# Kernel tuning notes

Measured on AMD Instinct MI355X. Metric: run time of the kernel, lower is better.

The kernel has to match this reference:

```python
import jax, jax.numpy as jnp
import numpy as np

DEGREE = 4  # standard ChebyKANLinear default -> 5 basis functions
LN_EPS = 1e-5


def cheby_basis(x, degree=DEGREE):
    # x: [N, D] -> basis [N, D, degree+1] of Chebyshev T_k(tanh(x))
    t = jnp.tanh(x)
    polys = [jnp.ones_like(t), t]
    for _ in range(2, degree + 1):
        polys.append(2.0 * t * polys[-1] - polys[-2])
    return jnp.stack(polys, axis=-1)


def cheby_kan_linear(x, coeffs):
    # coeffs: [in, out, degree+1]
    basis = cheby_basis(x)  # [N, in, degree+1]
    return jnp.einsum('nid,iod->no', basis, coeffs)


def layer_norm(x, gamma, beta):
    mu = jnp.mean(x, axis=-1, keepdims=True)
    var = jnp.mean(jnp.square(x - mu), axis=-1, keepdims=True)
    return (x - mu) * jax.lax.rsqrt(var + LN_EPS) * gamma + beta


def setup_inputs() -> dict:
    key = jax.random.key(0)
    ks = jax.random.split(key, 4)
    N, C, H = 262144, 128, 32
    scale1 = 1.0 / (C * (DEGREE + 1)) ** 0.5
    scale2 = 1.0 / (H * (DEGREE + 1)) ** 0.5
    return {
        'PRV_feat': jax.random.normal(ks[0], (N, C), dtype=jnp.float32),
        'PR_feat': jax.random.normal(ks[1], (N, C), dtype=jnp.float32),
        'coeffs1': jax.random.normal(ks[2], (C, H, DEGREE + 1), dtype=jnp.float32) * scale1,
        'ln_gamma': jnp.ones((H,), dtype=jnp.float32),
        'ln_beta': jnp.zeros((H,), dtype=jnp.float32),
        'coeffs2': jax.random.normal(ks[3], (H, 1, DEGREE + 1), dtype=jnp.float32) * scale2,
        'alpha': jnp.float32(0.5),
    }


def reference(PRV_feat, PR_feat, coeffs1, ln_gamma, ln_beta, coeffs2, alpha):
    # context encoder: ChebyKAN -> LayerNorm -> ReLU
    context = cheby_kan_linear(PR_feat, coeffs1)           # [N, H]
    context = jax.nn.relu(layer_norm(context, ln_gamma, ln_beta))
    # attention gate: ChebyKAN -> Sigmoid, [N, 1]
    attn = jax.nn.sigmoid(cheby_kan_linear(context, coeffs2))
    enhanced = PRV_feat * attn                              # broadcast over channels
    fused = alpha * enhanced + PRV_feat
    return fused
```

## Files before the change

### kernel.cpp

```cpp
#include <hip/hip_runtime.h>
#include <hip/hip_bf16.h>

#define C_DIM 128
#define H_DIM 32

typedef __attribute__((ext_vector_type(8))) short bf16x8;
typedef __attribute__((ext_vector_type(4))) float f32x4;

__device__ __forceinline__ float tanh_fast(float x) {
    float e = __expf(2.0f * x);
    return 1.0f - 2.0f * __builtin_amdgcn_rcpf(e + 1.0f);
}

__device__ __forceinline__ short f2bf(float f) {
    return __builtin_bit_cast(short, __float2bfloat16(f));
}

__global__ void prep_kernel(const float* __restrict__ c1, const float* __restrict__ c2,
                            unsigned short* __restrict__ Bpack, float* __restrict__ bias1,
                            float* __restrict__ E2, float* __restrict__ bias2) {
    const int tid = threadIdx.x;
    const int idx = blockIdx.x * 256 + tid;
    {
        int kc = idx >> 10;
        int oh = (idx >> 9) & 1;
        int l  = (idx >> 3) & 63;
        int j  = idx & 7;
        int g  = l >> 4;
        int kc2 = kc >> 1, kh = kc & 1;
        int c   = kc2 * 16 + 4 * g + 2 * kh + (j >> 2);
        int col = oh * 16 + (l & 15);
        int p   = j & 3;
        const float* cc = c1 + (c * H_DIM + col) * 5;
        float v = (p == 0) ? cc[1] - 3.0f * cc[3]
                : (p == 1) ? 2.0f * cc[2] - 8.0f * cc[4]
                : (p == 2) ? 4.0f * cc[3]
                           : 8.0f * cc[4];
        Bpack[idx] = (unsigned short)f2bf(v);
    }
    if (blockIdx.x == 0) {
        __shared__ float part[256];
        const int o = tid & 31, ch = tid >> 5;
        float b = 0.0f;
        for (int i = ch * 16; i < ch * 16 + 16; ++i) {
            const float* cc = c1 + (i * H_DIM + o) * 5;
            b += cc[0] - cc[2] + cc[4];
        }
        part[tid] = b;
        __syncthreads();
        if (tid < 32) {
            float s = 0.0f;
            #pragma unroll
            for (int k = 0; k < 8; ++k) s += part[k * 32 + tid];
            bias1[tid] = s;
            const float* cc = c2 + tid * 5;
            float4 e;
            e.x = cc[1] - 3.0f * cc[3];
            e.y = 2.0f * cc[2] - 8.0f * cc[4];
            e.z = 4.0f * cc[3];
            e.w = 8.0f * cc[4];
            reinterpret_cast<float4*>(E2)[tid] = e;
        }
        __syncthreads();
        if (tid < 32) part[tid] = c2[tid * 5] - c2[tid * 5 + 2] + c2[tid * 5 + 4];
        __syncthreads();
        if (tid == 0) {
            float b2 = 0.0f;
            for (int h = 0; h < 32; ++h) b2 += part[h];
            bias2[0] = b2;
        }
    }
}

__global__ __launch_bounds__(512, 4) void fused_kernel(
        const float* __restrict__ PRV, const float* __restrict__ PR,
        const unsigned short* __restrict__ Bpack, const float* __restrict__ bias1,
        const float* __restrict__ E2, const float* __restrict__ bias2,
        const float* __restrict__ gamma, const float* __restrict__ beta,
        const float* __restrict__ alphap, float* __restrict__ out) {
    __shared__ short sB[16 * 2 * 64 * 8];
    __shared__ float s_scale[256];

    const int tid  = threadIdx.x;
    const int wid  = tid >> 6;
    const int lane = tid & 63;
    const int g    = lane >> 4;
    const int lr   = lane & 15;

    const float4* pr4 = reinterpret_cast<const float4*>(PR);
    const size_t rbase = (size_t)blockIdx.x * 256 + wid * 32 + lr;
    const float4* q0 = pr4 + (rbase +  0) * (C_DIM / 4) + g;
    const float4* q1 = pr4 + (rbase + 16) * (C_DIM / 4) + g;

    float4 xa[8], xb[8];
    #pragma unroll
    for (int k = 0; k < 8; ++k) { xa[k] = q0[k * 4]; xb[k] = q1[k * 4]; }

    {
        const float4* src = reinterpret_cast<const float4*>(Bpack);
        float4* dst = reinterpret_cast<float4*>(sB);
        #pragma unroll
        for (int j = 0; j < 4; ++j) dst[j * 512 + tid] = src[j * 512 + tid];
    }
    __syncthreads();

    f32x4 acc[2][2];
    {
        float b0 = bias1[lr], b1 = bias1[16 + lr];
        #pragma unroll
        for (int t = 0; t < 2; ++t) {
            acc[t][0] = (f32x4){b0, b0, b0, b0};
            acc[t][1] = (f32x4){b1, b1, b1, b1};
        }
    }

    const bf16x8* sB8 = reinterpret_cast<const bf16x8*>(sB);

    #pragma unroll
    for (int kc2 = 0; kc2 < 8; ++kc2) {
        bf16x8 be0 = sB8[(kc2 * 4 + 0) * 64 + lane];
        bf16x8 be1 = sB8[(kc2 * 4 + 1) * 64 + lane];
        bf16x8 bo0 = sB8[(kc2 * 4 + 2) * 64 + lane];
        bf16x8 bo1 = sB8[(kc2 * 4 + 3) * 64 + lane];
        #define DO_TILE(XC, T) { \
            float t0 = tanh_fast(XC.x), t1 = tanh_fast(XC.y); \
            float t2 = tanh_fast(XC.z), t3 = tanh_fast(XC.w); \
            float s0 = t0 * t0, s1 = t1 * t1, s2 = t2 * t2, s3 = t3 * t3; \
            bf16x8 ae, ao; \
            ae[0] = f2bf(t0); ae[1] = f2bf(s0); ae[2] = f2bf(s0 * t0); ae[3] = f2bf(s0 * s0); \
            ae[4] = f2bf(t1); ae[5] = f2bf(s1); ae[6] = f2bf(s1 * t1); ae[7] = f2bf(s1 * s1); \
            ao[0] = f2bf(t2); ao[1] = f2bf(s2); ao[2] = f2bf(s2 * t2); ao[3] = f2bf(s2 * s2); \
            ao[4] = f2bf(t3); ao[5] = f2bf(s3); ao[6] = f2bf(s3 * t3); ao[7] = f2bf(s3 * s3); \
            acc[T][0] = __builtin_amdgcn_mfma_f32_16x16x32_bf16(ae, be0, acc[T][0], 0, 0, 0); \
            acc[T][1] = __builtin_amdgcn_mfma_f32_16x16x32_bf16(ae, be1, acc[T][1], 0, 0, 0); \
            acc[T][0] = __builtin_amdgcn_mfma_f32_16x16x32_bf16(ao, bo0, acc[T][0], 0, 0, 0); \
            acc[T][1] = __builtin_amdgcn_mfma_f32_16x16x32_bf16(ao, bo1, acc[T][1], 0, 0, 0); }
        DO_TILE(xa[kc2], 0)
        DO_TILE(xb[kc2], 1)
        #undef DO_TILE
    }

    const float gam0 = gamma[lr], gam1 = gamma[16 + lr];
    const float bet0 = beta[lr],  bet1 = beta[16 + lr];
    const float4 e2a = reinterpret_cast<const float4*>(E2)[lr];
    const float4 e2b = reinterpret_cast<const float4*>(E2)[16 + lr];
    const float zb = bias2[0];
    const float alpha = alphap[0];

    #pragma unroll
    for (int t = 0; t < 2; ++t) {
        f32x4 a0 = acc[t][0], a1 = acc[t][1];
        float s[4], vs[4], z[4];
        #pragma unroll
        for (int r = 0; r < 4; ++r) s[r] = a0[r] + a1[r];
        #pragma unroll
        for (int m = 1; m <= 8; m <<= 1) {
            #pragma unroll
            for (int r = 0; r < 4; ++r) s[r] += __shfl_xor(s[r], m, 64);
        }
        #pragma unroll
        for (int r = 0; r < 4; ++r) {
            float mu = s[r] * (1.0f / 32.0f);
            float d0 = a0[r] - mu, d1 = a1[r] - mu;
            a0[r] = d0; a1[r] = d1;
            vs[r] = d0 * d0 + d1 * d1;
        }
        #pragma unroll
        for (int m = 1; m <= 8; m <<= 1) {
            #pragma unroll
            for (int r = 0; r < 4; ++r) vs[r] += __shfl_xor(vs[r], m, 64);
        }
        #pragma unroll
        for (int r = 0; r < 4; ++r) {
            float rs = rsqrtf(vs[r] * (1.0f / 32.0f) + 1e-5f);
            float h0 = fmaf(a0[r] * rs, gam0, bet0);
            float h1 = fmaf(a1[r] * rs, gam1, bet1);
            h0 = fmaxf(h0, 0.0f); h1 = fmaxf(h1, 0.0f);
            float t0 = tanh_fast(h0), t1 = tanh_fast(h1);
            float t02 = t0 * t0, t12 = t1 * t1;
            float zp = fmaf(e2a.x, t0, fmaf(e2a.y, t02,
                        fmaf(e2a.z, t02 * t0, e2a.w * (t02 * t02))));
            zp += fmaf(e2b.x, t1, fmaf(e2b.y, t12,
                    fmaf(e2b.z, t12 * t1, e2b.w * (t12 * t12))));
            z[r] = zp;
        }
        #pragma unroll
        for (int m = 1; m <= 8; m <<= 1) {
            #pragma unroll
            for (int r = 0; r < 4; ++r) z[r] += __shfl_xor(z[r], m, 64);
        }
        if (lr == 0) {
            #pragma unroll
            for (int r = 0; r < 4; ++r) {
                float attn = __builtin_amdgcn_rcpf(1.0f + __expf(-(z[r] + zb)));
                s_scale[wid * 32 + t * 16 + g * 4 + r] = fmaf(alpha, attn, 1.0f);
            }
        }
    }
    __syncthreads();

    const size_t base = (size_t)blockIdx.x * 256 * (C_DIM / 4);
    const float4* prv4 = reinterpret_cast<const float4*>(PRV) + base;
    float4* out4 = reinterpret_cast<float4*>(out) + base;
    #pragma unroll 4
    for (int it = 0; it < 16; ++it) {
        int idx = it * 512 + tid;
        float sc = s_scale[idx >> 5];
        float4 v = prv4[idx];
        v.x *= sc; v.y *= sc; v.z *= sc; v.w *= sc;
        out4[idx] = v;
    }
}

extern "C" void kernel_launch(void* const* d_in, const int* in_sizes, int n_in,
                              void* d_out, int out_size, void* d_ws, size_t ws_size,
                              hipStream_t stream) {
    const float* PRV    = (const float*)d_in[0];
    const float* PR     = (const float*)d_in[1];
    const float* c1     = (const float*)d_in[2];
    const float* gamma  = (const float*)d_in[3];
    const float* beta   = (const float*)d_in[4];
    const float* c2     = (const float*)d_in[5];
    const float* alphap = (const float*)d_in[6];
    float* out = (float*)d_out;

    unsigned short* Bpack = (unsigned short*)d_ws;
    float* wsf   = (float*)((char*)d_ws + 32768);
    float* bias1 = wsf;
    float* E2    = wsf + 32;
    float* bias2 = wsf + 160;

    const int N = in_sizes[0] / C_DIM;

    hipLaunchKernelGGL(prep_kernel, dim3(64), dim3(256), 0, stream,
                       c1, c2, Bpack, bias1, E2, bias2);
    hipLaunchKernelGGL(fused_kernel, dim3(N / 256), dim3(512), 0, stream,
                       PRV, PR, Bpack, bias1, E2, bias2, gamma, beta, alphap, out);
}
```

Before: 87.42 us.

## Prefetch PRV rows per wave before LayerNorm and drop the final block barrier

Each wave now issues its 16 PRV float4 loads with inline asm before the LayerNorm and attention epilogue, then consumes them with staged s_waitcnt vmcnt waits and writes the scaled output. Because each wave only reads its own rows' scales from shared memory, the final __syncthreads is removed. PR loads move from a full up-front register prefetch into the MFMA loop, and the gamma, beta and E2 parameter loads are hoisted ahead of it. The aim is to hide PRV load latency behind the epilogue and to reduce register pressure. The cost is reliance on hand-counted vmcnt values, which on CDNA also count stores, and on the ordering of inline asm loads.

After: 87.11 us. Within noise of the previous version (-0.4%).

```diff
diff --git a/kernel.cpp b/kernel.cpp
--- a/kernel.cpp
+++ b/kernel.cpp
@@ -86,16 +86,13 @@
     const int lane = tid & 63;
     const int g    = lane >> 4;
     const int lr   = lane & 15;
+    const int hi   = lane >> 5;
 
     const float4* pr4 = reinterpret_cast<const float4*>(PR);
     const size_t rbase = (size_t)blockIdx.x * 256 + wid * 32 + lr;
     const float4* q0 = pr4 + (rbase +  0) * (C_DIM / 4) + g;
     const float4* q1 = pr4 + (rbase + 16) * (C_DIM / 4) + g;
 
-    float4 xa[8], xb[8];
-    #pragma unroll
-    for (int k = 0; k < 8; ++k) { xa[k] = q0[k * 4]; xb[k] = q1[k * 4]; }
-
     {
         const float4* src = reinterpret_cast<const float4*>(Bpack);
         float4* dst = reinterpret_cast<float4*>(sB);
@@ -104,6 +101,13 @@
     }
     __syncthreads();
 
+    const float gam0 = gamma[lr], gam1 = gamma[16 + lr];
+    const float bet0 = beta[lr],  bet1 = beta[16 + lr];
+    const float4 e2a = reinterpret_cast<const float4*>(E2)[lr];
+    const float4 e2b = reinterpret_cast<const float4*>(E2)[16 + lr];
+    const float zb = bias2[0];
+    const float alpha = alphap[0];
+
     f32x4 acc[2][2];
     {
         float b0 = bias1[lr], b1 = bias1[16 + lr];
@@ -118,6 +122,8 @@
 
     #pragma unroll
     for (int kc2 = 0; kc2 < 8; ++kc2) {
+        float4 x0 = q0[kc2 * 4];
+        float4 x1 = q1[kc2 * 4];
         bf16x8 be0 = sB8[(kc2 * 4 + 0) * 64 + lane];
         bf16x8 be1 = sB8[(kc2 * 4 + 1) * 64 + lane];
         bf16x8 bo0 = sB8[(kc2 * 4 + 2) * 64 + lane];
@@ -135,17 +141,22 @@
             acc[T][1] = __builtin_amdgcn_mfma_f32_16x16x32_bf16(ae, be1, acc[T][1], 0, 0, 0); \
             acc[T][0] = __builtin_amdgcn_mfma_f32_16x16x32_bf16(ao, bo0, acc[T][0], 0, 0, 0); \
             acc[T][1] = __builtin_amdgcn_mfma_f32_16x16x32_bf16(ao, bo1, acc[T][1], 0, 0, 0); }
-        DO_TILE(xa[kc2], 0)
-        DO_TILE(xb[kc2], 1)
+        DO_TILE(x0, 0)
+        DO_TILE(x1, 1)
         #undef DO_TILE
     }
 
-    const float gam0 = gamma[lr], gam1 = gamma[16 + lr];
-    const float bet0 = beta[lr],  bet1 = beta[16 + lr];
-    const float4 e2a = reinterpret_cast<const float4*>(E2)[lr];
-    const float4 e2b = reinterpret_cast<const float4*>(E2)[16 + lr];
-    const float zb = bias2[0];
-    const float alpha = alphap[0];
+    const f32x4* pvb = reinterpret_cast<const f32x4*>(PRV)
+                       + (size_t)blockIdx.x * 8192 + wid * 1024 + lane;
+    #define PVLD(IT) \
+        f32x4 pv##IT; \
+        asm volatile("global_load_dwordx4 %0, %1, off" \
+                     : "=v"(pv##IT) : "v"(pvb + IT * 64));
+    PVLD(0)  PVLD(1)  PVLD(2)  PVLD(3)
+    PVLD(4)  PVLD(5)  PVLD(6)  PVLD(7)
+    PVLD(8)  PVLD(9)  PVLD(10) PVLD(11)
+    PVLD(12) PVLD(13) PVLD(14) PVLD(15)
+    #undef PVLD
 
     #pragma unroll
     for (int t = 0; t < 2; ++t) {
@@ -197,19 +208,21 @@
             }
         }
     }
-    __syncthreads();
-
-    const size_t base = (size_t)blockIdx.x * 256 * (C_DIM / 4);
-    const float4* prv4 = reinterpret_cast<const float4*>(PRV) + base;
-    float4* out4 = reinterpret_cast<float4*>(out) + base;
-    #pragma unroll 4
-    for (int it = 0; it < 16; ++it) {
-        int idx = it * 512 + tid;
-        float sc = s_scale[idx >> 5];
-        float4 v = prv4[idx];
-        v.x *= sc; v.y *= sc; v.z *= sc; v.w *= sc;
-        out4[idx] = v;
-    }
+
+    const float* s_wave = s_scale + wid * 32;
+    f32x4* ob = reinterpret_cast<f32x4*>(out)
+                + (size_t)blockIdx.x * 8192 + wid * 1024 + lane;
+    #define PVUSE(IT, CNT) { \
+        asm volatile("s_waitcnt vmcnt(" #CNT ")" : "+v"(pv##IT)); \
+        float sc = s_wave[IT * 2 + hi]; \
+        f32x4 v = pv##IT; \
+        v[0] *= sc; v[1] *= sc; v[2] *= sc; v[3] *= sc; \
+        ob[IT * 64] = v; }
+    PVUSE(0, 15) PVUSE(1, 14) PVUSE(2, 13) PVUSE(3, 12)
+    PVUSE(4, 11) PVUSE(5, 10) PVUSE(6, 9)  PVUSE(7, 8)
+    PVUSE(8, 7)  PVUSE(9, 6)  PVUSE(10, 5) PVUSE(11, 4)
+    PVUSE(12, 3) PVUSE(13, 2) PVUSE(14, 1) PVUSE(15, 0)
+    #undef PVUSE
 }
 
 extern "C" void kernel_launch(void* const* d_in, const int* in_sizes, int n_in,
```

## Split fused kernel into scale computation and separate gating pass

Applied to the files above, without the earlier changes.

Splits the single fused kernel into two. The first computes per-row gate scales from PR and writes them to workspace. The second streams PRV, multiplies each row by its scale and writes the output, using a grid-stride layout hardcoded to 2048 blocks. PR loads also move from an upfront prefetch of all chunks into the MFMA loop, which lowers register pressure but may expose load latency. The split adds a kernel launch and a small scale round trip through memory, and gate_kernel's fixed indexing assumes N=262144.

Measured after the change: 108.9 us. +24.5%, slower.

```diff
diff --git a/kernel.cpp b/kernel.cpp
--- a/kernel.cpp
+++ b/kernel.cpp
@@ -72,12 +72,12 @@
     }
 }
 
-__global__ __launch_bounds__(512, 4) void fused_kernel(
-        const float* __restrict__ PRV, const float* __restrict__ PR,
+__global__ __launch_bounds__(512, 4) void scale_kernel(
+        const float* __restrict__ PR,
         const unsigned short* __restrict__ Bpack, const float* __restrict__ bias1,
         const float* __restrict__ E2, const float* __restrict__ bias2,
         const float* __restrict__ gamma, const float* __restrict__ beta,
-        const float* __restrict__ alphap, float* __restrict__ out) {
+        const float* __restrict__ alphap, float* __restrict__ scale_out) {
     __shared__ short sB[16 * 2 * 64 * 8];
     __shared__ float s_scale[256];
 
@@ -92,10 +92,6 @@
     const float4* q0 = pr4 + (rbase +  0) * (C_DIM / 4) + g;
     const float4* q1 = pr4 + (rbase + 16) * (C_DIM / 4) + g;
 
-    float4 xa[8], xb[8];
-    #pragma unroll
-    for (int k = 0; k < 8; ++k) { xa[k] = q0[k * 4]; xb[k] = q1[k * 4]; }
-
     {
         const float4* src = reinterpret_cast<const float4*>(Bpack);
         float4* dst = reinterpret_cast<float4*>(sB);
@@ -104,6 +100,13 @@
     }
     __syncthreads();
 
+    const float gam0 = gamma[lr], gam1 = gamma[16 + lr];
+    const float bet0 = beta[lr],  bet1 = beta[16 + lr];
+    const float4 e2a = reinterpret_cast<const float4*>(E2)[lr];
+    const float4 e2b = reinterpret_cast<const float4*>(E2)[16 + lr];
+    const float zb = bias2[0];
+    const float alpha = alphap[0];
+
     f32x4 acc[2][2];
     {
         float b0 = bias1[lr], b1 = bias1[16 + lr];
@@ -118,6 +121,8 @@
 
     #pragma unroll
     for (int kc2 = 0; kc2 < 8; ++kc2) {
+        float4 x0 = q0[kc2 * 4];
+        float4 x1 = q1[kc2 * 4];
         bf16x8 be0 = sB8[(kc2 * 4 + 0) * 64 + lane];
         bf16x8 be1 = sB8[(kc2 * 4 + 1) * 64 + lane];
         bf16x8 bo0 = sB8[(kc2 * 4 + 2) * 64 + lane];
@@ -135,17 +140,10 @@
             acc[T][1] = __builtin_amdgcn_mfma_f32_16x16x32_bf16(ae, be1, acc[T][1], 0, 0, 0); \
             acc[T][0] = __builtin_amdgcn_mfma_f32_16x16x32_bf16(ao, bo0, acc[T][0], 0, 0, 0); \
             acc[T][1] = __builtin_amdgcn_mfma_f32_16x16x32_bf16(ao, bo1, acc[T][1], 0, 0, 0); }
-        DO_TILE(xa[kc2], 0)
-        DO_TILE(xb[kc2], 1)
+        DO_TILE(x0, 0)
+        DO_TILE(x1, 1)
         #undef DO_TILE
     }
-
-    const float gam0 = gamma[lr], gam1 = gamma[16 + lr];
-    const float bet0 = beta[lr],  bet1 = beta[16 + lr];
-    const float4 e2a = reinterpret_cast<const float4*>(E2)[lr];
-    const float4 e2b = reinterpret_cast<const float4*>(E2)[16 + lr];
-    const float zb = bias2[0];
-    const float alpha = alphap[0];
 
     #pragma unroll
     for (int t = 0; t < 2; ++t) {
@@ -199,16 +197,22 @@
     }
     __syncthreads();
 
-    const size_t base = (size_t)blockIdx.x * 256 * (C_DIM / 4);
-    const float4* prv4 = reinterpret_cast<const float4*>(PRV) + base;
-    float4* out4 = reinterpret_cast<float4*>(out) + base;
-    #pragma unroll 4
+    if (tid < 256) scale_out[blockIdx.x * 256 + tid] = s_scale[tid];
+}
+
+__global__ __launch_bounds__(256) void gate_kernel(
+        const float* __restrict__ PRV, const float* __restrict__ scale,
+        float* __restrict__ out) {
+    const int tid = blockIdx.x * 256 + threadIdx.x;
+    const f32x4* in4 = reinterpret_cast<const f32x4*>(PRV);
+    f32x4* out4 = reinterpret_cast<f32x4*>(out);
+    #pragma unroll
     for (int it = 0; it < 16; ++it) {
-        int idx = it * 512 + tid;
-        float sc = s_scale[idx >> 5];
-        float4 v = prv4[idx];
-        v.x *= sc; v.y *= sc; v.z *= sc; v.w *= sc;
-        out4[idx] = v;
+        int i = tid + it * (2048 * 256);
+        float sc = scale[i >> 5];
+        f32x4 v = in4[i];
+        v[0] *= sc; v[1] *= sc; v[2] *= sc; v[3] *= sc;
+        out4[i] = v;
     }
 }
 
@@ -229,11 +233,14 @@
     float* bias1 = wsf;
     float* E2    = wsf + 32;
     float* bias2 = wsf + 160;
+    float* scale = wsf + 192;
 
     const int N = in_sizes[0] / C_DIM;
 
     hipLaunchKernelGGL(prep_kernel, dim3(64), dim3(256), 0, stream,
                        c1, c2, Bpack, bias1, E2, bias2);
-    hipLaunchKernelGGL(fused_kernel, dim3(N / 256), dim3(512), 0, stream,
-                       PRV, PR, Bpack, bias1, E2, bias2, gamma, beta, alphap, out);
-}
+    hipLaunchKernelGGL(scale_kernel, dim3(N / 256), dim3(512), 0, stream,
+                       PR, Bpack, bias1, E2, bias2, gamma, beta, alphap, scale);
+    hipLaunchKernelGGL(gate_kernel, dim3(2048), dim3(256), 0, stream,
+                       PRV, scale, out);
+}
```

## Stage PR tile through swizzled LDS and read B fragments from global

Applied to the files above, without the earlier changes.

The fused kernel now uses 256-thread blocks of 128 rows. Each block copies its whole PR tile into 64KB of XOR-swizzled shared memory with fully coalesced float4 loads, and each wave then reads its MFMA input rows from LDS. The packed B coefficients are read straight from global/L2 instead of being staged in LDS, and the per-row scale values reuse the PR staging buffer. The aim is better coalescing on the big PR read, but the 64KB LDS footprint limits occupancy and adds latency hiding risk.

Result: slower. 95.59 us (+9.3%).

```diff
diff --git a/kernel.cpp b/kernel.cpp
--- a/kernel.cpp
+++ b/kernel.cpp
@@ -72,14 +72,14 @@
     }
 }
 
-__global__ __launch_bounds__(512, 4) void fused_kernel(
+__global__ __launch_bounds__(256, 2) void fused_kernel(
         const float* __restrict__ PRV, const float* __restrict__ PR,
         const unsigned short* __restrict__ Bpack, const float* __restrict__ bias1,
         const float* __restrict__ E2, const float* __restrict__ bias2,
         const float* __restrict__ gamma, const float* __restrict__ beta,
         const float* __restrict__ alphap, float* __restrict__ out) {
-    __shared__ short sB[16 * 2 * 64 * 8];
-    __shared__ float s_scale[256];
+    __shared__ char smem[65536];
+    float* sPRf = reinterpret_cast<float*>(smem);
 
     const int tid  = threadIdx.x;
     const int wid  = tid >> 6;
@@ -87,22 +87,22 @@
     const int g    = lane >> 4;
     const int lr   = lane & 15;
 
-    const float4* pr4 = reinterpret_cast<const float4*>(PR);
-    const size_t rbase = (size_t)blockIdx.x * 256 + wid * 32 + lr;
-    const float4* q0 = pr4 + (rbase +  0) * (C_DIM / 4) + g;
-    const float4* q1 = pr4 + (rbase + 16) * (C_DIM / 4) + g;
-
-    float4 xa[8], xb[8];
+    const float4* prsrc = reinterpret_cast<const float4*>(PR) + (size_t)blockIdx.x * 4096;
     #pragma unroll
-    for (int k = 0; k < 8; ++k) { xa[k] = q0[k * 4]; xb[k] = q1[k * 4]; }
-
-    {
-        const float4* src = reinterpret_cast<const float4*>(Bpack);
-        float4* dst = reinterpret_cast<float4*>(sB);
-        #pragma unroll
-        for (int j = 0; j < 4; ++j) dst[j * 512 + tid] = src[j * 512 + tid];
+    for (int i = 0; i < 16; ++i) {
+        int fi  = i * 256 + tid;
+        int row = fi >> 5;
+        int ob  = ((fi & 31) * 16) ^ ((row & 7) << 4);
+        *reinterpret_cast<float4*>(smem + row * 512 + ob) = prsrc[fi];
     }
     __syncthreads();
+
+    const float gam0 = gamma[lr], gam1 = gamma[16 + lr];
+    const float bet0 = beta[lr],  bet1 = beta[16 + lr];
+    const f32x4 e2a = reinterpret_cast<const f32x4*>(E2)[lr];
+    const f32x4 e2b = reinterpret_cast<const f32x4*>(E2)[16 + lr];
+    const float zb = bias2[0];
+    const float alpha = alphap[0];
 
     f32x4 acc[2][2];
     {
@@ -114,17 +114,23 @@
         }
     }
 
-    const bf16x8* sB8 = reinterpret_cast<const bf16x8*>(sB);
+    const bf16x8* Bg = reinterpret_cast<const bf16x8*>(Bpack);
+    const int rA = wid * 32 + lr;
+    const int rB = rA + 16;
+    const int swz = (lr & 7) << 4;
 
     #pragma unroll
     for (int kc2 = 0; kc2 < 8; ++kc2) {
-        bf16x8 be0 = sB8[(kc2 * 4 + 0) * 64 + lane];
-        bf16x8 be1 = sB8[(kc2 * 4 + 1) * 64 + lane];
-        bf16x8 bo0 = sB8[(kc2 * 4 + 2) * 64 + lane];
-        bf16x8 bo1 = sB8[(kc2 * 4 + 3) * 64 + lane];
+        const int o = kc2 * 64 + g * 16;
+        f32x4 x0 = *reinterpret_cast<const f32x4*>(smem + rA * 512 + (o ^ swz));
+        f32x4 x1 = *reinterpret_cast<const f32x4*>(smem + rB * 512 + (o ^ swz));
+        bf16x8 be0 = Bg[(kc2 * 4 + 0) * 64 + lane];
+        bf16x8 be1 = Bg[(kc2 * 4 + 1) * 64 + lane];
+        bf16x8 bo0 = Bg[(kc2 * 4 + 2) * 64 + lane];
+        bf16x8 bo1 = Bg[(kc2 * 4 + 3) * 64 + lane];
         #define DO_TILE(XC, T) { \
-            float t0 = tanh_fast(XC.x), t1 = tanh_fast(XC.y); \
-            float t2 = tanh_fast(XC.z), t3 = tanh_fast(XC.w); \
+            float t0 = tanh_fast(XC[0]), t1 = tanh_fast(XC[1]); \
+            float t2 = tanh_fast(XC[2]), t3 = tanh_fast(XC[3]); \
             float s0 = t0 * t0, s1 = t1 * t1, s2 = t2 * t2, s3 = t3 * t3; \
             bf16x8 ae, ao; \
             ae[0] = f2bf(t0); ae[1] = f2bf(s0); ae[2] = f2bf(s0 * t0); ae[3] = f2bf(s0 * s0); \
@@ -135,17 +141,10 @@
             acc[T][1] = __builtin_amdgcn_mfma_f32_16x16x32_bf16(ae, be1, acc[T][1], 0, 0, 0); \
             acc[T][0] = __builtin_amdgcn_mfma_f32_16x16x32_bf16(ao, bo0, acc[T][0], 0, 0, 0); \
             acc[T][1] = __builtin_amdgcn_mfma_f32_16x16x32_bf16(ao, bo1, acc[T][1], 0, 0, 0); }
-        DO_TILE(xa[kc2], 0)
-        DO_TILE(xb[kc2], 1)
+        DO_TILE(x0, 0)
+        DO_TILE(x1, 1)
         #undef DO_TILE
     }
-
-    const float gam0 = gamma[lr], gam1 = gamma[16 + lr];
-    const float bet0 = beta[lr],  bet1 = beta[16 + lr];
-    const float4 e2a = reinterpret_cast<const float4*>(E2)[lr];
-    const float4 e2b = reinterpret_cast<const float4*>(E2)[16 + lr];
-    const float zb = bias2[0];
-    const float alpha = alphap[0];
 
     #pragma unroll
     for (int t = 0; t < 2; ++t) {
@@ -178,10 +177,10 @@
             h0 = fmaxf(h0, 0.0f); h1 = fmaxf(h1, 0.0f);
             float t0 = tanh_fast(h0), t1 = tanh_fast(h1);
             float t02 = t0 * t0, t12 = t1 * t1;
-            float zp = fmaf(e2a.x, t0, fmaf(e2a.y, t02,
-                        fmaf(e2a.z, t02 * t0, e2a.w * (t02 * t02))));
-            zp += fmaf(e2b.x, t1, fmaf(e2b.y, t12,
-                    fmaf(e2b.z, t12 * t1, e2b.w * (t12 * t12))));
+            float zp = fmaf(e2a[0], t0, fmaf(e2a[1], t02,
+                        fmaf(e2a[2], t02 * t0, e2a[3] * (t02 * t02))));
+            zp += fmaf(e2b[0], t1, fmaf(e2b[1], t12,
+                    fmaf(e2b[2], t12 * t1, e2b[3] * (t12 * t12))));
             z[r] = zp;
         }
         #pragma unroll
@@ -193,19 +192,20 @@
             #pragma unroll
             for (int r = 0; r < 4; ++r) {
                 float attn = __builtin_amdgcn_rcpf(1.0f + __expf(-(z[r] + zb)));
-                s_scale[wid * 32 + t * 16 + g * 4 + r] = fmaf(alpha, attn, 1.0f);
+                sPRf[wid * 4096 + t * 16 + g * 4 + r] = fmaf(alpha, attn, 1.0f);
             }
         }
     }
     __syncthreads();
 
-    const size_t base = (size_t)blockIdx.x * 256 * (C_DIM / 4);
+    const size_t base = (size_t)blockIdx.x * 4096;
     const float4* prv4 = reinterpret_cast<const float4*>(PRV) + base;
     float4* out4 = reinterpret_cast<float4*>(out) + base;
     #pragma unroll 4
     for (int it = 0; it < 16; ++it) {
-        int idx = it * 512 + tid;
-        float sc = s_scale[idx >> 5];
+        int idx = it * 256 + tid;
+        int R = idx >> 5;
+        float sc = sPRf[(R >> 5) * 4096 + (R & 31)];
         float4 v = prv4[idx];
         v.x *= sc; v.y *= sc; v.z *= sc; v.w *= sc;
         out4[idx] = v;
@@ -234,6 +234,6 @@
 
     hipLaunchKernelGGL(prep_kernel, dim3(64), dim3(256), 0, stream,
                        c1, c2, Bpack, bias1, E2, bias2);
-    hipLaunchKernelGGL(fused_kernel, dim3(N / 256), dim3(512), 0, stream,
+    hipLaunchKernelGGL(fused_kernel, dim3(N / 128), dim3(256), 0, stream,
                        PRV, PR, Bpack, bias1, E2, bias2, gamma, beta, alphap, out);
 }
```
